# Performance work log

Measured on AMD Instinct MI355X. Metric: run time of the kernel, lower is better.

The kernel has to match this reference:

```python
import jax, jax.numpy as jnp
import numpy as np

M = 4  # num_modals
EPS = 1e-6


def setup_inputs() -> dict:
    key = jax.random.key(0)
    ks = jax.random.split(key, 12)
    c, h, r, B, n = 768, 3072, 16, 4, 1024
    inp = {
        "x": jax.random.normal(ks[0], (M * B, n, c), jnp.float32),
        "fc1_w": jax.random.normal(ks[1], (h, c), jnp.float32) * 0.02,
        "fc1_b": jax.random.normal(ks[2], (h,), jnp.float32) * 0.02,
        "fc2_w": jax.random.normal(ks[3], (c, h), jnp.float32) * 0.02,
        "fc2_b": jax.random.normal(ks[4], (c,), jnp.float32) * 0.02,
        "a_fc1": jax.random.normal(ks[5], (M, r, c), jnp.float32) * 0.02,
        "b_fc1": jax.random.normal(ks[6], (M, h, r), jnp.float32) * 0.02,
        "a_fc2": jax.random.normal(ks[7], (M, r, h), jnp.float32) * 0.02,
        "b_fc2": jax.random.normal(ks[8], (M, c, r), jnp.float32) * 0.02,
        "gate_w": jax.random.normal(ks[9], (M, M, c), jnp.float32) * 0.02,
        "gate_b": jax.random.normal(ks[10], (M, M), jnp.float32) * 0.02,
        "modality_mask": jax.random.randint(ks[11], (M, B), 0, 2, jnp.int32),
    }
    return inp


def _fused_combine(rw, mask_f, lora):
    # rw: [M,B,n,M] routing softmax; mask_f: [M,B]; lora: [M,B,n,d]
    # per_routing_weights[i,j,t,k] = rw[i,j,t,k] * mask[k,j], renormalized over k
    masked = rw * mask_f.T[None, :, None, :]                      # [M,B,n,M]
    norm = masked / (jnp.sum(masked, axis=-1, keepdims=True) + EPS)
    fused = jnp.einsum("ibnk,kbnd->ibnd", norm, lora)             # combine experts
    return fused * mask_f[:, :, None, None]                       # rows with mask==0 stay zero


def reference(x, fc1_w, fc1_b, fc2_w, fc2_b, a_fc1, b_fc1, a_fc2, b_fc2,
              gate_w, gate_b, modality_mask):
    bs_m, n, c = x.shape
    B = bs_m // M
    xm = x.reshape(M, B, n, c)
    mask_f = modality_mask.astype(x.dtype)                        # [M,B]

    # base fc1
    x1 = (jnp.einsum("ibnc,hc->ibnh", xm, fc1_w) + fc1_b)         # [M,B,n,h]

    # per-modality routing softmax over M experts (computed in fp32 as in torch)
    logits = jnp.einsum("ibnc,iec->ibne", xm, gate_w) + gate_b[:, None, None, :]
    rw = jax.nn.softmax(logits.astype(jnp.float32), axis=-1).astype(x.dtype)

    # HiRA delta for fc1: elementwise(fc1_w, B@A) per modality
    delta1 = fc1_w[None] * jnp.einsum("ihr,irc->ihc", b_fc1, a_fc1)  # [M,h,c]
    lora1 = jnp.einsum("ibnc,ihc->ibnh", xm, delta1)              # [M,B,n,h]

    x1 = x1 + _fused_combine(rw, mask_f, lora1)
    x1 = jax.nn.gelu(x1, approximate=False)                       # mlp.act

    # base fc2
    x2 = jnp.einsum("ibnh,ch->ibnc", x1, fc2_w) + fc2_b           # [M,B,n,c]

    # HiRA delta for fc2
    delta2 = fc2_w[None] * jnp.einsum("icr,irh->ich", b_fc2, a_fc2)  # [M,c,h]
    lora2 = jnp.einsum("ibnh,ich->ibnc", x1, delta2)              # [M,B,n,c]

    x2 = x2 + _fused_combine(rw, mask_f, lora2)
    return x2.reshape(bs_m, n, c)
```

## Files before the change

kernel.cpp:

```cpp
#include <hip/hip_runtime.h>
#include <hip/hip_bf16.h>
#include <math.h>

#define NMOD 4
#define NB 4
#define NTOKN 1024
#define CDIM 768
#define HDIM 3072
#define RDIM 16
#define MROWS (NMOD*NB*NTOKN)
#define RPM (NB*NTOKN)

typedef __bf16 bf16_t;
typedef __bf16 bf16x4 __attribute__((ext_vector_type(4)));
typedef __bf16 bf16x8 __attribute__((ext_vector_type(8)));
typedef float f32x4 __attribute__((ext_vector_type(4)));

__global__ void cvt_kernel(const float* __restrict__ in, bf16_t* __restrict__ out, int n) {
  int i = (blockIdx.x * blockDim.x + threadIdx.x) * 4;
  if (i >= n) return;
  const float4 v = *reinterpret_cast<const float4*>(in + i);
  bf16x4 o;
  o[0] = (bf16_t)v.x; o[1] = (bf16_t)v.y; o[2] = (bf16_t)v.z; o[3] = (bf16_t)v.w;
  *reinterpret_cast<bf16x4*>(out + i) = o;
}

__global__ void delta1_kernel(const float* __restrict__ fc1w, const float* __restrict__ a1,
                              const float* __restrict__ b1, bf16_t* __restrict__ out) {
  int idx = blockIdx.x * blockDim.x + threadIdx.x;
  if (idx >= NMOD*HDIM*CDIM) return;
  int c = idx % CDIM;
  int h = (idx / CDIM) % HDIM;
  int k = idx / (CDIM*HDIM);
  const float* brow = b1 + ((size_t)k*HDIM + h)*RDIM;
  const float* acol = a1 + (size_t)k*RDIM*CDIM + c;
  float s = 0.f;
  #pragma unroll
  for (int r = 0; r < RDIM; ++r) s += brow[r] * acol[r*CDIM];
  out[idx] = (bf16_t)(fc1w[h*CDIM + c] * s);
}

__global__ void delta2_kernel(const float* __restrict__ fc2w, const float* __restrict__ a2,
                              const float* __restrict__ b2, bf16_t* __restrict__ out) {
  int idx = blockIdx.x * blockDim.x + threadIdx.x;
  if (idx >= NMOD*CDIM*HDIM) return;
  int h = idx % HDIM;
  int c = (idx / HDIM) % CDIM;
  int k = idx / (HDIM*CDIM);
  const float* brow = b2 + ((size_t)k*CDIM + c)*RDIM;
  const float* acol = a2 + (size_t)k*RDIM*HDIM + h;
  float s = 0.f;
  #pragma unroll
  for (int r = 0; r < RDIM; ++r) s += brow[r] * acol[r*HDIM];
  out[idx] = (bf16_t)(fc2w[c*HDIM + h] * s);
}

__global__ void gate_kernel(const float* __restrict__ x, const float* __restrict__ gw,
                            const float* __restrict__ gb, const int* __restrict__ mask,
                            float* __restrict__ normw, bf16_t* __restrict__ x_bf) {
  int t = blockIdx.x * 4 + (threadIdx.x >> 6);
  int lane = threadIdx.x & 63;
  int i = t >> 12;
  int b = (t >> 10) & 3;
  const float* xr = x + (size_t)t * CDIM;
  bf16_t* xo = x_bf + (size_t)t * CDIM;
  float acc[NMOD] = {0.f, 0.f, 0.f, 0.f};
  for (int c = lane; c < CDIM; c += 64) {
    float xv = xr[c];
    xo[c] = (bf16_t)xv;
    #pragma unroll
    for (int e = 0; e < NMOD; ++e) acc[e] += xv * gw[(i*NMOD + e)*CDIM + c];
  }
  #pragma unroll
  for (int e = 0; e < NMOD; ++e) {
    float v = acc[e];
    #pragma unroll
    for (int off = 32; off > 0; off >>= 1) v += __shfl_xor(v, off);
    acc[e] = v;
  }
  if (lane == 0) {
    float lg[NMOD], mx = -1e30f;
    #pragma unroll
    for (int e = 0; e < NMOD; ++e) { lg[e] = acc[e] + gb[i*NMOD + e]; mx = fmaxf(mx, lg[e]); }
    float s = 0.f;
    #pragma unroll
    for (int e = 0; e < NMOD; ++e) { lg[e] = expf(lg[e] - mx); s += lg[e]; }
    float inv = 1.f / s;
    float num[NMOD], den = 0.f;
    #pragma unroll
    for (int k = 0; k < NMOD; ++k) {
      float mk = (float)mask[k*NB + b];
      num[k] = lg[k] * inv * mk;
      den += num[k];
    }
    float mi = (float)mask[i*NB + b];
    float scale = mi / (den + 1e-6f);
    #pragma unroll
    for (int k = 0; k < NMOD; ++k) normw[(size_t)t*4 + k] = num[k] * scale;
  }
}

#define BMT 128
#define BNT 128
#define BKT 64

__device__ __forceinline__ void gload_lds16(const bf16_t* g, bf16_t* l) {
  __builtin_amdgcn_global_load_lds((const __attribute__((address_space(1))) void*)g,
                                   (__attribute__((address_space(3))) void*)l, 16, 0, 0);
}
#define MFMA_BF16 __builtin_amdgcn_mfma_f32_16x16x32_bf16

__global__ __launch_bounds__(256, 2)
void gemm_kernel(const bf16_t* __restrict__ A, const bf16_t* __restrict__ W0,
                 const bf16_t* __restrict__ WL, const float* __restrict__ bias,
                 const int* __restrict__ mask,
                 bf16_t* __restrict__ outB, bf16_t* __restrict__ outL,
                 int K, int N, int P, int modStride, int rowOff, int posOff) {
  __shared__ __align__(16) bf16_t As[BMT * BKT];
  __shared__ __align__(16) bf16_t Bs[BNT * BKT];

  const int tid  = threadIdx.x;
  const int lane = tid & 63;
  const int wv   = tid >> 6;
  const int wr   = wv >> 1, wc = wv & 1;
  const int row0 = blockIdx.x * BMT;
  const int col0 = blockIdx.y * BNT;
  const bool lora = (blockIdx.z != 0);

  const int mod = row0 / P;
  if (lora) {
    const int bb = (posOff + (row0 % P)) >> 10;
    if (mask[mod*NB + bb] == 0) return;
  }
  const int gArow0 = mod * modStride + rowOff + (row0 % P);
  const bf16_t* Wp = lora ? (WL + (size_t)mod * N * K) : W0;

  const int ldr = tid >> 3;
  const int ssl = ((tid & 7) ^ (ldr & 7)) * 8;
  const bf16_t* Ag = A  + (size_t)(gArow0 + ldr) * K + ssl;
  const bf16_t* Wg = Wp + (size_t)(col0   + ldr) * K + ssl;

  const int fr  = lane & 15;
  const int hi  = lane >> 4;
  const int sk0 = ((hi)     ^ (fr & 7)) * 8;
  const int sk1 = ((4 + hi) ^ (fr & 7)) * 8;

  f32x4 acc[4][4];
  #pragma unroll
  for (int i = 0; i < 4; ++i)
    #pragma unroll
    for (int j = 0; j < 4; ++j) acc[i][j] = (f32x4){0.f, 0.f, 0.f, 0.f};

  for (int k0 = 0; k0 < K; k0 += BKT) {
    __syncthreads();
    #pragma unroll
    for (int j = 0; j < 4; ++j)
      gload_lds16(Ag + (size_t)(j*32) * K + k0, &As[tid*8 + j*2048]);
    #pragma unroll
    for (int j = 0; j < 4; ++j)
      gload_lds16(Wg + (size_t)(j*32) * K + k0, &Bs[tid*8 + j*2048]);
    __syncthreads();

    #pragma unroll
    for (int kk = 0; kk < 2; ++kk) {
      const int sk = (kk == 0) ? sk0 : sk1;
      bf16x8 af[4], bfr[4];
      #pragma unroll
      for (int mi = 0; mi < 4; ++mi)
        af[mi] = *reinterpret_cast<const bf16x8*>(&As[(wr*64 + mi*16 + fr)*BKT + sk]);
      #pragma unroll
      for (int ni = 0; ni < 4; ++ni)
        bfr[ni] = *reinterpret_cast<const bf16x8*>(&Bs[(wc*64 + ni*16 + fr)*BKT + sk]);
      #pragma unroll
      for (int mi = 0; mi < 4; ++mi)
        #pragma unroll
        for (int ni = 0; ni < 4; ++ni)
          acc[mi][ni] = MFMA_BF16(af[mi], bfr[ni], acc[mi][ni], 0, 0, 0);
    }
  }

  bf16_t* outp = lora ? outL : outB;
  #pragma unroll
  for (int mi = 0; mi < 4; ++mi) {
    #pragma unroll
    for (int ni = 0; ni < 4; ++ni) {
      const int colg = col0 + wc*64 + ni*16 + fr;
      float bv = 0.f;
      if (!lora) bv = bias[colg];
      #pragma unroll
      for (int rg = 0; rg < 4; ++rg) {
        const int rowg = row0 + wr*64 + mi*16 + hi*4 + rg;
        outp[(size_t)rowg * N + colg] = (bf16_t)(acc[mi][ni][rg] + bv);
      }
    }
  }
}

__global__ void combine1_kernel(bf16_t* __restrict__ base1, const bf16_t* __restrict__ L1,
                                const float* __restrict__ normw, int P, int chunkOff) {
  int idx = blockIdx.x * blockDim.x + threadIdx.x;
  if (idx >= P * (HDIM/8)) return;
  int h0 = (idx % (HDIM/8)) * 8;
  int p  = idx / (HDIM/8);
  float lv[4][8];
  #pragma unroll
  for (int k = 0; k < 4; ++k) {
    bf16x8 v = *reinterpret_cast<const bf16x8*>(&L1[((size_t)(k*P + p))*HDIM + h0]);
    #pragma unroll
    for (int j = 0; j < 8; ++j) lv[k][j] = (float)v[j];
  }
  #pragma unroll
  for (int i = 0; i < 4; ++i) {
    size_t ro = ((size_t)(i*P + p))*HDIM + h0;
    const float* nw = normw + ((size_t)(i*RPM + chunkOff + p))*4;
    float n0 = nw[0], n1 = nw[1], n2 = nw[2], n3 = nw[3];
    bf16x8 bv = *reinterpret_cast<const bf16x8*>(&base1[ro]);
    bf16x8 ov;
    #pragma unroll
    for (int j = 0; j < 8; ++j) {
      float v = (float)bv[j] + n0*lv[0][j] + n1*lv[1][j] + n2*lv[2][j] + n3*lv[3][j];
      float g = 0.5f * v * (1.f + erff(v * 0.70710678118654752f));
      ov[j] = (bf16_t)g;
    }
    *reinterpret_cast<bf16x8*>(&base1[ro]) = ov;
  }
}

__global__ void combine2_kernel(const bf16_t* __restrict__ base2, const bf16_t* __restrict__ L2,
                                const float* __restrict__ normw, float* __restrict__ out,
                                int P, int chunkOff) {
  int idx = blockIdx.x * blockDim.x + threadIdx.x;
  if (idx >= P * (CDIM/8)) return;
  int c0 = (idx % (CDIM/8)) * 8;
  int p  = idx / (CDIM/8);
  float lv[4][8];
  #pragma unroll
  for (int k = 0; k < 4; ++k) {
    bf16x8 v = *reinterpret_cast<const bf16x8*>(&L2[((size_t)(k*P + p))*CDIM + c0]);
    #pragma unroll
    for (int j = 0; j < 8; ++j) lv[k][j] = (float)v[j];
  }
  #pragma unroll
  for (int i = 0; i < 4; ++i) {
    int grow = i*RPM + chunkOff + p;
    const float* nw = normw + (size_t)grow*4;
    float n0 = nw[0], n1 = nw[1], n2 = nw[2], n3 = nw[3];
    bf16x8 bv = *reinterpret_cast<const bf16x8*>(&base2[((size_t)(i*P + p))*CDIM + c0]);
    float o[8];
    #pragma unroll
    for (int j = 0; j < 8; ++j)
      o[j] = (float)bv[j] + n0*lv[0][j] + n1*lv[1][j] + n2*lv[2][j] + n3*lv[3][j];
    float4* op = reinterpret_cast<float4*>(out + (size_t)grow*CDIM + c0);
    op[0] = make_float4(o[0], o[1], o[2], o[3]);
    op[1] = make_float4(o[4], o[5], o[6], o[7]);
  }
}

extern "C" void kernel_launch(void* const* d_in, const int* in_sizes, int n_in,
                              void* d_out, int out_size, void* d_ws, size_t ws_size,
                              hipStream_t stream) {
  (void)in_sizes; (void)n_in; (void)out_size;
  const float* x    = (const float*)d_in[0];
  const float* fc1w = (const float*)d_in[1];
  const float* fc1b = (const float*)d_in[2];
  const float* fc2w = (const float*)d_in[3];
  const float* fc2b = (const float*)d_in[4];
  const float* a1   = (const float*)d_in[5];
  const float* b1   = (const float*)d_in[6];
  const float* a2   = (const float*)d_in[7];
  const float* b2   = (const float*)d_in[8];
  const float* gw   = (const float*)d_in[9];
  const float* gb   = (const float*)d_in[10];
  const int*   mask = (const int*)d_in[11];
  float* out = (float*)d_out;

  char* ws = (char*)d_ws;
  size_t off = 0;
  auto carve = [&](size_t bytes) -> char* {
    char* p = ws + off; off += (bytes + 255) & ~(size_t)255; return p;
  };
  bf16_t* x_bf  = (bf16_t*)carve((size_t)MROWS*CDIM*2);
  bf16_t* w1_bf = (bf16_t*)carve((size_t)HDIM*CDIM*2);
  bf16_t* w2_bf = (bf16_t*)carve((size_t)CDIM*HDIM*2);
  bf16_t* d1_bf = (bf16_t*)carve((size_t)NMOD*HDIM*CDIM*2);
  bf16_t* d2_bf = (bf16_t*)carve((size_t)NMOD*CDIM*HDIM*2);
  float*  normw = (float*)carve((size_t)MROWS*4*4);
  const size_t fixedBytes = off;

  int P = RPM;
  while (P > 128 && fixedBytes + (size_t)61440*P + 4096 > ws_size) P >>= 1;
  const int NCH = RPM / P;

  bf16_t* base1 = (bf16_t*)carve((size_t)NMOD*P*HDIM*2);
  bf16_t* L1    = (bf16_t*)carve((size_t)NMOD*P*HDIM*2);
  bf16_t* base2 = (bf16_t*)carve((size_t)NMOD*P*CDIM*2);
  bf16_t* L2    = (bf16_t*)carve((size_t)NMOD*P*CDIM*2);

  cvt_kernel<<<HDIM*CDIM/1024, 256, 0, stream>>>(fc1w, w1_bf, HDIM*CDIM);
  cvt_kernel<<<CDIM*HDIM/1024, 256, 0, stream>>>(fc2w, w2_bf, CDIM*HDIM);
  delta1_kernel<<<NMOD*HDIM*CDIM/256, 256, 0, stream>>>(fc1w, a1, b1, d1_bf);
  delta2_kernel<<<NMOD*CDIM*HDIM/256, 256, 0, stream>>>(fc2w, a2, b2, d2_bf);
  gate_kernel<<<MROWS/4, 256, 0, stream>>>(x, gw, gb, mask, normw, x_bf);

  for (int g = 0; g < NCH; ++g) {
    const int chunkOff = g * P;
    gemm_kernel<<<dim3(NMOD*P/BMT, HDIM/BNT, 2), 256, 0, stream>>>(
        x_bf, w1_bf, d1_bf, fc1b, mask, base1, L1, CDIM, HDIM, P, RPM, chunkOff, chunkOff);
    combine1_kernel<<<(P*(HDIM/8) + 255)/256, 256, 0, stream>>>(base1, L1, normw, P, chunkOff);
    gemm_kernel<<<dim3(NMOD*P/BMT, CDIM/BNT, 2), 256, 0, stream>>>(
        base1, w2_bf, d2_bf, fc2b, mask, base2, L2, HDIM, CDIM, P, P, 0, chunkOff);
    combine2_kernel<<<(P*(CDIM/8) + 255)/256, 256, 0, stream>>>(base2, L2, normw, out, P, chunkOff);
  }
}
```

Measured before the change: 481.9 us.

## Double-buffer GEMM LDS tiles and skip masked LoRA reads in combine kernels

```diff
diff --git a/kernel.cpp b/kernel.cpp
--- a/kernel.cpp
+++ b/kernel.cpp
@@ -116,8 +116,7 @@
                  const int* __restrict__ mask,
                  bf16_t* __restrict__ outB, bf16_t* __restrict__ outL,
                  int K, int N, int P, int modStride, int rowOff, int posOff) {
-  __shared__ __align__(16) bf16_t As[BMT * BKT];
-  __shared__ __align__(16) bf16_t Bs[BNT * BKT];
+  __shared__ __align__(16) bf16_t lds[2][2][BMT * BKT];
 
   const int tid  = threadIdx.x;
   const int lane = tid & 63;
@@ -140,6 +139,16 @@
   const bf16_t* Ag = A  + (size_t)(gArow0 + ldr) * K + ssl;
   const bf16_t* Wg = Wp + (size_t)(col0   + ldr) * K + ssl;
 
+#define STAGE(buf, t) do {                                                      \
+    const int ko_ = (t)*BKT;                                                    \
+    _Pragma("unroll")                                                           \
+    for (int j_ = 0; j_ < 4; ++j_)                                              \
+      gload_lds16(Ag + (size_t)(j_*32)*K + ko_, &lds[buf][0][tid*8 + j_*2048]); \
+    _Pragma("unroll")                                                           \
+    for (int j_ = 0; j_ < 4; ++j_)                                              \
+      gload_lds16(Wg + (size_t)(j_*32)*K + ko_, &lds[buf][1][tid*8 + j_*2048]); \
+  } while (0)
+
   const int fr  = lane & 15;
   const int hi  = lane >> 4;
   const int sk0 = ((hi)     ^ (fr & 7)) * 8;
@@ -151,15 +160,16 @@
     #pragma unroll
     for (int j = 0; j < 4; ++j) acc[i][j] = (f32x4){0.f, 0.f, 0.f, 0.f};
 
-  for (int k0 = 0; k0 < K; k0 += BKT) {
-    __syncthreads();
-    #pragma unroll
-    for (int j = 0; j < 4; ++j)
-      gload_lds16(Ag + (size_t)(j*32) * K + k0, &As[tid*8 + j*2048]);
-    #pragma unroll
-    for (int j = 0; j < 4; ++j)
-      gload_lds16(Wg + (size_t)(j*32) * K + k0, &Bs[tid*8 + j*2048]);
-    __syncthreads();
+  const int NT = K / BKT;
+
+  STAGE(0, 0);
+  __syncthreads();
+
+  int buf = 0;
+  for (int t = 0; t < NT; ++t) {
+    if (t + 1 < NT) STAGE(buf ^ 1, t + 1);
+    const bf16_t* As_ = &lds[buf][0][0];
+    const bf16_t* Bs_ = &lds[buf][1][0];
 
     #pragma unroll
     for (int kk = 0; kk < 2; ++kk) {
@@ -167,17 +177,20 @@
       bf16x8 af[4], bfr[4];
       #pragma unroll
       for (int mi = 0; mi < 4; ++mi)
-        af[mi] = *reinterpret_cast<const bf16x8*>(&As[(wr*64 + mi*16 + fr)*BKT + sk]);
+        af[mi] = *reinterpret_cast<const bf16x8*>(&As_[(wr*64 + mi*16 + fr)*BKT + sk]);
       #pragma unroll
       for (int ni = 0; ni < 4; ++ni)
-        bfr[ni] = *reinterpret_cast<const bf16x8*>(&Bs[(wc*64 + ni*16 + fr)*BKT + sk]);
+        bfr[ni] = *reinterpret_cast<const bf16x8*>(&Bs_[(wc*64 + ni*16 + fr)*BKT + sk]);
       #pragma unroll
       for (int mi = 0; mi < 4; ++mi)
         #pragma unroll
         for (int ni = 0; ni < 4; ++ni)
           acc[mi][ni] = MFMA_BF16(af[mi], bfr[ni], acc[mi][ni], 0, 0, 0);
     }
-  }
+    __syncthreads();
+    buf ^= 1;
+  }
+#undef STAGE
 
   bf16_t* outp = lora ? outL : outB;
   #pragma unroll
@@ -197,17 +210,24 @@
 }
 
 __global__ void combine1_kernel(bf16_t* __restrict__ base1, const bf16_t* __restrict__ L1,
-                                const float* __restrict__ normw, int P, int chunkOff) {
+                                const float* __restrict__ normw, const int* __restrict__ mask,
+                                int P, int chunkOff) {
   int idx = blockIdx.x * blockDim.x + threadIdx.x;
   if (idx >= P * (HDIM/8)) return;
   int h0 = (idx % (HDIM/8)) * 8;
   int p  = idx / (HDIM/8);
+  const int b = (chunkOff + p) >> 10;
   float lv[4][8];
   #pragma unroll
   for (int k = 0; k < 4; ++k) {
-    bf16x8 v = *reinterpret_cast<const bf16x8*>(&L1[((size_t)(k*P + p))*HDIM + h0]);
-    #pragma unroll
-    for (int j = 0; j < 8; ++j) lv[k][j] = (float)v[j];
+    if (mask[k*NB + b] != 0) {
+      bf16x8 v = *reinterpret_cast<const bf16x8*>(&L1[((size_t)(k*P + p))*HDIM + h0]);
+      #pragma unroll
+      for (int j = 0; j < 8; ++j) lv[k][j] = (float)v[j];
+    } else {
+      #pragma unroll
+      for (int j = 0; j < 8; ++j) lv[k][j] = 0.f;
+    }
   }
   #pragma unroll
   for (int i = 0; i < 4; ++i) {
@@ -227,18 +247,24 @@
 }
 
 __global__ void combine2_kernel(const bf16_t* __restrict__ base2, const bf16_t* __restrict__ L2,
-                                const float* __restrict__ normw, float* __restrict__ out,
-                                int P, int chunkOff) {
+                                const float* __restrict__ normw, const int* __restrict__ mask,
+                                float* __restrict__ out, int P, int chunkOff) {
   int idx = blockIdx.x * blockDim.x + threadIdx.x;
   if (idx >= P * (CDIM/8)) return;
   int c0 = (idx % (CDIM/8)) * 8;
   int p  = idx / (CDIM/8);
+  const int b = (chunkOff + p) >> 10;
   float lv[4][8];
   #pragma unroll
   for (int k = 0; k < 4; ++k) {
-    bf16x8 v = *reinterpret_cast<const bf16x8*>(&L2[((size_t)(k*P + p))*CDIM + c0]);
-    #pragma unroll
-    for (int j = 0; j < 8; ++j) lv[k][j] = (float)v[j];
+    if (mask[k*NB + b] != 0) {
+      bf16x8 v = *reinterpret_cast<const bf16x8*>(&L2[((size_t)(k*P + p))*CDIM + c0]);
+      #pragma unroll
+      for (int j = 0; j < 8; ++j) lv[k][j] = (float)v[j];
+    } else {
+      #pragma unroll
+      for (int j = 0; j < 8; ++j) lv[k][j] = 0.f;
+    }
   }
   #pragma unroll
   for (int i = 0; i < 4; ++i) {
@@ -306,9 +332,9 @@
     const int chunkOff = g * P;
     gemm_kernel<<<dim3(NMOD*P/BMT, HDIM/BNT, 2), 256, 0, stream>>>(
         x_bf, w1_bf, d1_bf, fc1b, mask, base1, L1, CDIM, HDIM, P, RPM, chunkOff, chunkOff);
-    combine1_kernel<<<(P*(HDIM/8) + 255)/256, 256, 0, stream>>>(base1, L1, normw, P, chunkOff);
+    combine1_kernel<<<(P*(HDIM/8) + 255)/256, 256, 0, stream>>>(base1, L1, normw, mask, P, chunkOff);
     gemm_kernel<<<dim3(NMOD*P/BMT, CDIM/BNT, 2), 256, 0, stream>>>(
         base1, w2_bf, d2_bf, fc2b, mask, base2, L2, HDIM, CDIM, P, P, 0, chunkOff);
-    combine2_kernel<<<(P*(CDIM/8) + 255)/256, 256, 0, stream>>>(base2, L2, normw, out, P, chunkOff);
-  }
-}
+    combine2_kernel<<<(P*(CDIM/8) + 255)/256, 256, 0, stream>>>(base2, L2, normw, mask, out, P, chunkOff);
+  }
+}
```

New measurement: 507.6 us. 5.3% more time.
